# Optimization experiments

Measured on AMD Instinct MI355X. Metric: run time of the kernel, lower is better.

The kernel has to match this reference:

```python
import jax, jax.numpy as jnp
import numpy as np

N = 50000; E = 800000; B = 5000
ND = 32; ED = 16; HD = 64; H = 128; L = 3
IN_DIM = ND + 2 * H  # 288, GNN in_channels
NEG = 0.2  # GATv2 leaky_relu slope
EPS = 1e-5  # LayerNorm eps


def silu(x):
    return x * jax.nn.sigmoid(x)


def layer_norm(x, g, b):
    mu = jnp.mean(x, -1, keepdims=True)
    v = jnp.var(x, -1, keepdims=True)
    return (x - mu) * jax.lax.rsqrt(v + EPS) * g + b


def setup_inputs() -> dict:
    key = jax.random.key(0)
    ks = iter(jax.random.split(key, 48))

    def w(shape):
        return jax.random.normal(next(ks), shape, jnp.float32) * 0.02

    inp = {}
    inp['x_t'] = jax.random.normal(next(ks), (N, ND), jnp.float32)
    inp['t'] = jax.random.randint(next(ks), (N,), 0, 1000)
    inp['household_features'] = jax.random.normal(next(ks), (B, HD), jnp.float32)
    inp['edge_index'] = jax.random.randint(next(ks), (2, E), 0, N)
    inp['edge_attr'] = jax.random.normal(next(ks), (E, ED), jnp.float32)
    inp['batch'] = jnp.sort(jax.random.randint(next(ks), (N,), 0, B))
    z = jnp.zeros; o = jnp.ones
    inp.update(dict(
        tW1=w((1, H)), tb1=z(H), tW2=w((H, H)), tb2=z(H),
        hW1=w((HD, H)), hb1=z(H), hg1=o(H), hB1=z(H),
        hW2=w((H, H)), hb2=z(H), hg2=o(H), hB2=z(H),
        Wl=w((L, IN_DIM, H)), bl=z((L, H)), Wr=w((L, IN_DIM, H)), br=z((L, H)),
        We=w((L, ED, H)), att=w((L, H)), gb=z((L, H)),
        fcpW=w((H, IN_DIM)), fcpb=z(IN_DIM),
        npW1=w((H, H)), npb1=z(H), npg=o(H), npB=z(H),
        npW2=w((H, ND)), npb2=z(ND)))
    return inp


def reference(x_t, t, household_features, edge_index, edge_attr, batch,
              tW1, tb1, tW2, tb2,
              hW1, hb1, hg1, hB1, hW2, hb2, hg2, hB2,
              Wl, bl, Wr, br, We, att, gb,
              fcpW, fcpb, npW1, npb1, npg, npB, npW2, npb2):
    # time embedding: Linear(1,H) -> SiLU -> Linear(H,H)
    t_emb = silu(t[:, None].astype(jnp.float32) @ tW1 + tb1) @ tW2 + tb2
    # household encoder: (Linear, LN, SiLU) x2, then gather per node
    h = silu(layer_norm(household_features @ hW1 + hb1, hg1, hB1))
    h = silu(layer_norm(h @ hW2 + hb2, hg2, hB2))
    x = jnp.concatenate([x_t, t_emb, h[batch]], axis=1)  # [N, IN_DIM]

    # add self loops (PyG default), edge_attr filled with per-feature mean
    loop = jnp.arange(N)
    src = jnp.concatenate([edge_index[0], loop])
    dst = jnp.concatenate([edge_index[1], loop])
    ea = jnp.concatenate([edge_attr, jnp.broadcast_to(edge_attr.mean(0), (N, ED))], axis=0)

    for l in range(L):  # GATv2Conv layers (heads=1)
        xl = x @ Wl[l] + bl[l]  # [N, H] source transform
        xr = x @ Wr[l] + br[l]  # [N, H] target transform
        m = jax.nn.leaky_relu(xl[src] + xr[dst] + ea @ We[l], NEG)  # [Etot, H]
        score = m @ att[l]  # [Etot]
        smax = jax.ops.segment_max(score, dst, num_segments=N)
        ex = jnp.exp(score - smax[dst])
        denom = jax.ops.segment_sum(ex, dst, num_segments=N) + 1e-16
        alpha = ex / denom[dst]
        out = jax.ops.segment_sum(alpha[:, None] * xl[src], dst, num_segments=N) + gb[l]
        x = silu(out)
        if l < L - 1:
            x = x @ fcpW + fcpb  # fc_projection back to IN_DIM
    # node_projection: Linear, LN, SiLU, Linear
    return silu(layer_norm(x @ npW1 + npb1, npg, npB)) @ npW2 + npb2
```

## Files before the change

kernel.cpp:

```cpp
#include <hip/hip_runtime.h>
#include <hip/hip_bf16.h>

#define NN 50000
#define NE 800000
#define NB 5000
#define ND 32
#define EDD 16
#define HDD 64
#define H 128
#define ETOT (NE + NN)
#define NEG 0.2f
#define EPS_LN 1e-5f

__device__ __forceinline__ float siluf(float x){ return x / (1.f + __expf(-x)); }

__device__ __forceinline__ float wsum(float v){
  v += __shfl_xor(v, 32, 64);
  v += __shfl_xor(v, 16, 64);
  v += __shfl_xor(v, 8, 64);
  v += __shfl_xor(v, 4, 64);
  v += __shfl_xor(v, 2, 64);
  v += __shfl_xor(v, 1, 64);
  return v;
}

__device__ __forceinline__ float blockLN128(float x, const float* g, const float* b, int j, float* red){
  int lane = j & 63, wid = j >> 6;
  float s = wsum(x);
  if (lane == 0) red[wid] = s;
  __syncthreads();
  float mu = (red[0] + red[1]) * 0.0078125f;
  float d = x - mu;
  float s2 = wsum(d * d);
  if (lane == 0) red[2 + wid] = s2;
  __syncthreads();
  float var = (red[2] + red[3]) * 0.0078125f;
  return d * (1.f / sqrtf(var + EPS_LN)) * g[j] + b[j];
}

__global__ __launch_bounds__(128) void k_house(const float* __restrict__ hf,
    const float* __restrict__ hW1, const float* __restrict__ hb1,
    const float* __restrict__ hg1, const float* __restrict__ hB1,
    const float* __restrict__ hW2, const float* __restrict__ hb2,
    const float* __restrict__ hg2, const float* __restrict__ hB2,
    float* __restrict__ hout){
  __shared__ float sin_[HDD];
  __shared__ float smid[H];
  __shared__ float red[4];
  int bidx = blockIdx.x, j = threadIdx.x;
  if (j < HDD) sin_[j] = hf[bidx * HDD + j];
  __syncthreads();
  float acc = hb1[j];
  #pragma unroll
  for (int k = 0; k < HDD; k++) acc += sin_[k] * hW1[k * H + j];
  float v = siluf(blockLN128(acc, hg1, hB1, j, red));
  __syncthreads();
  smid[j] = v;
  __syncthreads();
  float acc2 = hb2[j];
  #pragma unroll
  for (int k = 0; k < H; k++) acc2 += smid[k] * hW2[k * H + j];
  float v2 = siluf(blockLN128(acc2, hg2, hB2, j, red));
  hout[bidx * H + j] = v2;
}

__global__ __launch_bounds__(128) void k_temb(const float* __restrict__ tW1, const float* __restrict__ tb1,
    const float* __restrict__ tW2, const float* __restrict__ tb2, float* __restrict__ table){
  __shared__ float smid[H];
  int bidx = blockIdx.x, j = threadIdx.x;
  float tv = (float)bidx;
  smid[j] = siluf(tv * tW1[j] + tb1[j]);
  __syncthreads();
  float acc = tb2[j];
  #pragma unroll
  for (int k = 0; k < H; k++) acc += smid[k] * tW2[k * H + j];
  table[bidx * H + j] = acc;
}

__global__ __launch_bounds__(256) void k_gemm(const float* __restrict__ A, const float* __restrict__ W,
    const float* __restrict__ bias, float* __restrict__ C, int M, int K, int Nc){
  __shared__ float As[16][68];
  __shared__ float Ws[16][64];
  int t = threadIdx.x;
  int m0 = blockIdx.x * 64, n0 = blockIdx.y * 64;
  int tx = t & 15, ty = t >> 4;
  int la_m = t >> 2, la_k = (t & 3) << 2;
  int lw_k = t >> 4, lw_j = (t & 15) << 2;
  float acc[4][4] = {{0.f}};
  int arow = m0 + la_m;
  for (int k0 = 0; k0 < K; k0 += 16){
    float4 a = make_float4(0.f, 0.f, 0.f, 0.f);
    if (arow < M) a = *(const float4*)(A + (size_t)arow * K + k0 + la_k);
    As[la_k + 0][la_m] = a.x; As[la_k + 1][la_m] = a.y;
    As[la_k + 2][la_m] = a.z; As[la_k + 3][la_m] = a.w;
    float4 wv = make_float4(0.f, 0.f, 0.f, 0.f);
    if (n0 + lw_j < Nc) wv = *(const float4*)(W + (size_t)(k0 + lw_k) * Nc + n0 + lw_j);
    *(float4*)&Ws[lw_k][lw_j] = wv;
    __syncthreads();
    #pragma unroll
    for (int k = 0; k < 16; k++){
      float4 a4 = *(const float4*)&As[k][ty << 2];
      float4 b4 = *(const float4*)&Ws[k][tx << 2];
      acc[0][0] += a4.x * b4.x; acc[0][1] += a4.x * b4.y; acc[0][2] += a4.x * b4.z; acc[0][3] += a4.x * b4.w;
      acc[1][0] += a4.y * b4.x; acc[1][1] += a4.y * b4.y; acc[1][2] += a4.y * b4.z; acc[1][3] += a4.y * b4.w;
      acc[2][0] += a4.z * b4.x; acc[2][1] += a4.z * b4.y; acc[2][2] += a4.z * b4.z; acc[2][3] += a4.z * b4.w;
      acc[3][0] += a4.w * b4.x; acc[3][1] += a4.w * b4.y; acc[3][2] += a4.w * b4.z; acc[3][3] += a4.w * b4.w;
    }
    __syncthreads();
  }
  int col = n0 + (tx << 2);
  if (col < Nc){
    float4 b4 = make_float4(0.f, 0.f, 0.f, 0.f);
    if (bias) b4 = *(const float4*)(bias + col);
    #pragma unroll
    for (int r = 0; r < 4; r++){
      int row = m0 + (ty << 2) + r;
      if (row < M){
        float4 o = make_float4(acc[r][0] + b4.x, acc[r][1] + b4.y, acc[r][2] + b4.z, acc[r][3] + b4.w);
        *(float4*)(C + (size_t)row * Nc + col) = o;
      }
    }
  }
}

__global__ __launch_bounds__(256) void k_gemm128(const float* __restrict__ A, const float* __restrict__ W,
    const float* __restrict__ bias, float* __restrict__ C, int M, int K, int Nc){
  __shared__ float As[16][132];
  __shared__ float Ws[16][128];
  int t = threadIdx.x;
  int m0 = blockIdx.x * 128, n0 = blockIdx.y * 128;
  int tx = t & 15, ty = t >> 4;
  float acc[8][8];
  #pragma unroll
  for (int r = 0; r < 8; r++)
    #pragma unroll
    for (int c = 0; c < 8; c++) acc[r][c] = 0.f;
  for (int k0 = 0; k0 < K; k0 += 16){
    #pragma unroll
    for (int l = 0; l < 2; l++){
      int idx = t + l * 256;
      int ar = idx >> 2, ac = (idx & 3) << 2;
      float4 a = make_float4(0.f, 0.f, 0.f, 0.f);
      if (m0 + ar < M) a = *(const float4*)(A + (size_t)(m0 + ar) * K + k0 + ac);
      As[ac + 0][ar] = a.x; As[ac + 1][ar] = a.y;
      As[ac + 2][ar] = a.z; As[ac + 3][ar] = a.w;
    }
    #pragma unroll
    for (int l = 0; l < 2; l++){
      int idx = t + l * 256;
      int wr = idx >> 5, wc = (idx & 31) << 2;
      float4 wv = make_float4(0.f, 0.f, 0.f, 0.f);
      if (n0 + wc < Nc) wv = *(const float4*)(W + (size_t)(k0 + wr) * Nc + n0 + wc);
      *(float4*)&Ws[wr][wc] = wv;
    }
    __syncthreads();
    #pragma unroll
    for (int k = 0; k < 16; k++){
      float4 a0 = *(const float4*)&As[k][ty * 8];
      float4 a1 = *(const float4*)&As[k][ty * 8 + 4];
      float4 b0 = *(const float4*)&Ws[k][tx * 8];
      float4 b1 = *(const float4*)&Ws[k][tx * 8 + 4];
      float ar_[8] = {a0.x, a0.y, a0.z, a0.w, a1.x, a1.y, a1.z, a1.w};
      float bc_[8] = {b0.x, b0.y, b0.z, b0.w, b1.x, b1.y, b1.z, b1.w};
      #pragma unroll
      for (int r = 0; r < 8; r++)
        #pragma unroll
        for (int c = 0; c < 8; c++) acc[r][c] += ar_[r] * bc_[c];
    }
    __syncthreads();
  }
  int col = n0 + tx * 8;
  float4 bb0 = make_float4(0.f, 0.f, 0.f, 0.f), bb1 = bb0;
  if (bias && col < Nc){ bb0 = *(const float4*)(bias + col); bb1 = *(const float4*)(bias + col + 4); }
  #pragma unroll
  for (int r = 0; r < 8; r++){
    int row = m0 + ty * 8 + r;
    if (row < M && col < Nc){
      float4 o0 = make_float4(acc[r][0] + bb0.x, acc[r][1] + bb0.y, acc[r][2] + bb0.z, acc[r][3] + bb0.w);
      float4 o1 = make_float4(acc[r][4] + bb1.x, acc[r][5] + bb1.y, acc[r][6] + bb1.z, acc[r][7] + bb1.w);
      *(float4*)(C + (size_t)row * Nc + col) = o0;
      *(float4*)(C + (size_t)row * Nc + col + 4) = o1;
    }
  }
}

__global__ void k_pack0(const float* __restrict__ Wl, const float* __restrict__ Wr,
    float* __restrict__ Whead, float* __restrict__ Wmid, float* __restrict__ Wtail){
  int r = blockIdx.x, c = threadIdx.x;
  float v = (c < H) ? Wl[r * H + c] : Wr[r * H + (c - H)];
  if (r < 32) Whead[r * 256 + c] = v;
  else if (r < 160) Wmid[(r - 32) * 256 + c] = v;
  else Wtail[(r - 160) * 256 + c] = v;
}
__global__ void k_packW(const float* __restrict__ Wl, const float* __restrict__ Wr, float* __restrict__ Wp){
  int r = blockIdx.x, c = threadIdx.x;
  Wp[r * 256 + c] = (c < H) ? Wl[r * H + c] : Wr[r * H + (c - H)];
}
__global__ void k_bias0(const float* __restrict__ bl, const float* __restrict__ br, float* __restrict__ b0){
  int c = threadIdx.x;
  b0[c] = (c < H) ? bl[c] : br[c - H];
}
__global__ void k_cvec(const float* __restrict__ fcpb, const float* __restrict__ Wp,
    const float* __restrict__ bl, const float* __restrict__ br, float* __restrict__ cc){
  int c = threadIdx.x;
  float acc = (c < H) ? bl[c] : br[c - H];
  for (int k = 0; k < 288; k++) acc += fcpb[k] * Wp[k * 256 + c];
  cc[c] = acc;
}

__global__ __launch_bounds__(256) void k_xlr0(const float* __restrict__ x_t, const int* __restrict__ t,
    const int* __restrict__ batch, const float* __restrict__ T0, const float* __restrict__ H0,
    const float* __restrict__ Whead, const float* __restrict__ b0, float* __restrict__ xlr){
  __shared__ float sx[ND];
  __shared__ int sti, sbi;
  int i = blockIdx.x, c = threadIdx.x;
  if (c < ND) sx[c] = x_t[i * ND + c];
  if (c == 0){ sti = t[i]; sbi = batch[i]; }
  __syncthreads();
  float acc = b0[c] + T0[(size_t)sti * 256 + c] + H0[(size_t)sbi * 256 + c];
  #pragma unroll
  for (int k = 0; k < ND; k++) acc += sx[k] * Whead[k * 256 + c];
  xlr[(size_t)i * 256 + c] = acc;
}

__global__ void k_edge_mean(const float* __restrict__ ea, float* __restrict__ sum16){
  __shared__ float ss[16];
  int t = threadIdx.x;
  if (t < 16) ss[t] = 0.f;
  __syncthreads();
  float p[16];
  #pragma unroll
  for (int k = 0; k < 16; k++) p[k] = 0.f;
  for (int r = blockIdx.x * blockDim.x + t; r < NE; r += gridDim.x * blockDim.x){
    const float4* rp = (const float4*)(ea + (size_t)r * 16);
    float4 q0 = rp[0], q1 = rp[1], q2 = rp[2], q3 = rp[3];
    p[0] += q0.x; p[1] += q0.y; p[2] += q0.z; p[3] += q0.w;
    p[4] += q1.x; p[5] += q1.y; p[6] += q1.z; p[7] += q1.w;
    p[8] += q2.x; p[9] += q2.y; p[10] += q2.z; p[11] += q2.w;
    p[12] += q3.x; p[13] += q3.y; p[14] += q3.z; p[15] += q3.w;
  }
  #pragma unroll
  for (int k = 0; k < 16; k++) atomicAdd(&ss[k], p[k]);
  __syncthreads();
  if (t < 16) atomicAdd(&sum16[t], ss[t]);
}
__global__ void k_mean_scale(float* sum16){
  sum16[threadIdx.x] *= (1.f / NE);
}

__global__ void k_deg_init(int* __restrict__ deg){
  int i = blockIdx.x * 256 + threadIdx.x;
  if (i < NN) deg[i] = 1;
}
__global__ void k_deg_count(const int* __restrict__ eidx, int* __restrict__ deg){
  int e = blockIdx.x * 256 + threadIdx.x;
  if (e < NE) atomicAdd(&deg[eidx[NE + e]], 1);
}
__global__ __launch_bounds__(256) void k_scan1(const int* __restrict__ deg, int* __restrict__ row_ptr, int* __restrict__ bs){
  __shared__ int sc[256];
  int t = threadIdx.x;
  int base = blockIdx.x * 1024 + t * 4;
  int v0 = (base + 0 < NN) ? deg[base + 0] : 0;
  int v1 = (base + 1 < NN) ? deg[base + 1] : 0;
  int v2 = (base + 2 < NN) ? deg[base + 2] : 0;
  int v3 = (base + 3 < NN) ? deg[base + 3] : 0;
  int s0 = v0, s1 = s0 + v1, s2 = s1 + v2, s3 = s2 + v3;
  sc[t] = s3;
  __syncthreads();
  for (int off = 1; off < 256; off <<= 1){
    int add = (t >= off) ? sc[t - off] : 0;
    __syncthreads();
    sc[t] += add;
    __syncthreads();
  }
  int excl = sc[t] - s3;
  if (base + 0 < NN) row_ptr[base + 1] = excl + s0;
  if (base + 1 < NN) row_ptr[base + 2] = excl + s1;
  if (base + 2 < NN) row_ptr[base + 3] = excl + s2;
  if (base + 3 < NN) row_ptr[base + 4] = excl + s3;
  if (t == 255) bs[blockIdx.x] = sc[255];
}
__global__ void k_scan2(int* __restrict__ bs, int nb){
  int lane = threadIdx.x;
  int v = (lane < nb) ? bs[lane] : 0;
  for (int off = 1; off < 64; off <<= 1){
    int n = __shfl_up(v, off, 64);
    if (lane >= off) v += n;
  }
  if (lane < nb) bs[lane] = v;
}
__global__ void k_scan3(int* __restrict__ row_ptr, const int* __restrict__ bs){
  int i = blockIdx.x * 256 + threadIdx.x;
  if (i == 0) row_ptr[0] = 0;
  if (i < NN){
    int chunk = i >> 10;
    if (chunk > 0) row_ptr[i + 1] += bs[chunk - 1];
  }
}
__global__ void k_fill_init(const int* __restrict__ row_ptr, int* __restrict__ fill){
  int i = blockIdx.x * 256 + threadIdx.x;
  if (i < NN) fill[i] = row_ptr[i];
}
__global__ void k_fill_edges(const int* __restrict__ eidx, int* __restrict__ fill,
    int* __restrict__ csrc, int* __restrict__ ceid){
  int e = blockIdx.x * 256 + threadIdx.x;
  if (e < NE){
    int d = eidx[NE + e];
    int pos = atomicAdd(&fill[d], 1);
    csrc[pos] = eidx[e];
    ceid[pos] = e;
  }
}
__global__ void k_fill_self(int* __restrict__ fill, int* __restrict__ csrc, int* __restrict__ ceid){
  int i = blockIdx.x * 256 + threadIdx.x;
  if (i < NN){
    int pos = atomicAdd(&fill[i], 1);
    csrc[pos] = i;
    ceid[pos] = NE;
  }
}

__global__ __launch_bounds__(256) void k_sagg(const float* __restrict__ xlr,
    const float* __restrict__ ea, const float* __restrict__ eamean,
    const float* __restrict__ Wel, const float* __restrict__ attl, const float* __restrict__ gbl,
    const int* __restrict__ row_ptr, const int* __restrict__ csrc, const int* __restrict__ ceid,
    float* __restrict__ y){
  int t = threadIdx.x;
  int wid = t >> 6, lane = t & 63;
  int i = blockIdx.x * 4 + wid;
  if (i >= NN) return;
  int dim = lane << 1;
  float2 rW[16];
  #pragma unroll
  for (int k = 0; k < 16; k++) rW[k] = *(const float2*)(Wel + k * H + dim);
  float2 xr = *(const float2*)(xlr + (size_t)i * 256 + H + dim);
  float a0 = attl[dim], a1 = attl[dim + 1];
  int row = __builtin_amdgcn_readfirstlane(row_ptr[i]);
  int end = __builtin_amdgcn_readfirstlane(row_ptr[i + 1]);
  float m = -1e30f, den = 0.f, ax = 0.f, ay = 0.f;
  int s_c = __builtin_amdgcn_readfirstlane(csrc[row]);
  int e_c = __builtin_amdgcn_readfirstlane(ceid[row]);
  float2 vl_c = *(const float2*)(xlr + (size_t)s_c * 256 + dim);
  const float* ep_c = (e_c < NE) ? (ea + (size_t)e_c * 16) : eamean;
  float4 q0 = *(const float4*)(ep_c);
  float4 q1 = *(const float4*)(ep_c + 4);
  float4 q2 = *(const float4*)(ep_c + 8);
  float4 q3 = *(const float4*)(ep_c + 12);
  for (int p = row; p < end; ++p){
    int pn = (p + 1 < end) ? (p + 1) : p;
    int s_n = __builtin_amdgcn_readfirstlane(csrc[pn]);
    int e_n = __builtin_amdgcn_readfirstlane(ceid[pn]);
    float2 vl_n = *(const float2*)(xlr + (size_t)s_n * 256 + dim);
    const float* ep_n = (e_n < NE) ? (ea + (size_t)e_n * 16) : eamean;
    float4 n0 = *(const float4*)(ep_n);
    float4 n1 = *(const float4*)(ep_n + 4);
    float4 n2 = *(const float4*)(ep_n + 8);
    float4 n3 = *(const float4*)(ep_n + 12);
    float eav[16] = {q0.x, q0.y, q0.z, q0.w, q1.x, q1.y, q1.z, q1.w,
                     q2.x, q2.y, q2.z, q2.w, q3.x, q3.y, q3.z, q3.w};
    float ew0 = 0.f, ew1 = 0.f;
    #pragma unroll
    for (int k = 0; k < 16; k++){ ew0 += eav[k] * rW[k].x; ew1 += eav[k] * rW[k].y; }
    float vx = vl_c.x + xr.x + ew0;
    float vy = vl_c.y + xr.y + ew1;
    vx = fmaxf(vx, NEG * vx);
    vy = fmaxf(vy, NEG * vy);
    float sc = wsum(a0 * vx + a1 * vy);
    if (sc <= m){
      float wv = __expf(sc - m);
      den += wv; ax += wv * vl_c.x; ay += wv * vl_c.y;
    } else {
      float scale = __expf(m - sc);
      den = den * scale + 1.f;
      ax = ax * scale + vl_c.x;
      ay = ay * scale + vl_c.y;
      m = sc;
    }
    vl_c = vl_n; q0 = n0; q1 = n1; q2 = n2; q3 = n3;
  }
  float inv = 1.f / (den + 1e-16f);
  float ox = siluf(ax * inv + gbl[dim]);
  float oy = siluf(ay * inv + gbl[dim + 1]);
  *(float2*)(y + (size_t)i * H + dim) = make_float2(ox, oy);
}

__global__ __launch_bounds__(128) void k_ln_silu(const float* __restrict__ z, const float* __restrict__ g,
    const float* __restrict__ b, float* __restrict__ z2){
  __shared__ float red[4];
  int i = blockIdx.x, j = threadIdx.x;
  float x = z[(size_t)i * H + j];
  float v = blockLN128(x, g, b, j, red);
  z2[(size_t)i * H + j] = siluf(v);
}

extern "C" void kernel_launch(void* const* d_in, const int* in_sizes, int n_in,
                              void* d_out, int out_size, void* d_ws, size_t ws_size,
                              hipStream_t stream){
  (void)in_sizes; (void)n_in; (void)out_size; (void)ws_size;
  const float* x_t  = (const float*)d_in[0];
  const int*   t    = (const int*)d_in[1];
  const float* hf   = (const float*)d_in[2];
  const int*   eidx = (const int*)d_in[3];
  const float* ea   = (const float*)d_in[4];
  const int*   batch= (const int*)d_in[5];
  const float* tW1  = (const float*)d_in[6];
  const float* tb1  = (const float*)d_in[7];
  const float* tW2  = (const float*)d_in[8];
  const float* tb2  = (const float*)d_in[9];
  const float* hW1  = (const float*)d_in[10];
  const float* hb1  = (const float*)d_in[11];
  const float* hg1  = (const float*)d_in[12];
  const float* hB1  = (const float*)d_in[13];
  const float* hW2  = (const float*)d_in[14];
  const float* hb2  = (const float*)d_in[15];
  const float* hg2  = (const float*)d_in[16];
  const float* hB2  = (const float*)d_in[17];
  const float* Wl   = (const float*)d_in[18];
  const float* bl   = (const float*)d_in[19];
  const float* Wr   = (const float*)d_in[20];
  const float* br   = (const float*)d_in[21];
  const float* We   = (const float*)d_in[22];
  const float* att  = (const float*)d_in[23];
  const float* gb   = (const float*)d_in[24];
  const float* fcpW = (const float*)d_in[25];
  const float* fcpb = (const float*)d_in[26];
  const float* npW1 = (const float*)d_in[27];
  const float* npb1 = (const float*)d_in[28];
  const float* npg  = (const float*)d_in[29];
  const float* npB  = (const float*)d_in[30];
  const float* npW2 = (const float*)d_in[31];
  const float* npb2 = (const float*)d_in[32];

  char* w = (char*)d_ws;
  size_t off = 0;
  auto alloc = [&](size_t bytes) -> void* {
    void* p = w + off;
    off += (bytes + 255) & ~(size_t)255;
    return p;
  };
  float* table = (float*)alloc((size_t)1000 * H * 4);
  float* hbuf  = (float*)alloc((size_t)NB * H * 4);
  float* T0    = (float*)alloc((size_t)1000 * 256 * 4);
  float* H0b   = (float*)alloc((size_t)NB * 256 * 4);
  float* W0h   = (float*)alloc((size_t)32 * 256 * 4);
  float* W0m   = (float*)alloc((size_t)128 * 256 * 4);
  float* W0t   = (float*)alloc((size_t)128 * 256 * 4);
  float* b0    = (float*)alloc(256 * 4);
  float* Wp1   = (float*)alloc((size_t)288 * 256 * 4);
  float* Wp2   = (float*)alloc((size_t)288 * 256 * 4);
  float* Ac1   = (float*)alloc((size_t)128 * 256 * 4);
  float* Ac2   = (float*)alloc((size_t)128 * 256 * 4);
  float* cc1   = (float*)alloc(256 * 4);
  float* cc2   = (float*)alloc(256 * 4);
  float* eam   = (float*)alloc(16 * 4);
  int* deg     = (int*)alloc((size_t)NN * 4);
  int* row_ptr = (int*)alloc((size_t)(NN + 1) * 4);
  int* fill    = (int*)alloc((size_t)NN * 4);
  int* bs      = (int*)alloc(64 * 4);
  int* csrc    = (int*)alloc((size_t)ETOT * 4);
  int* ceid    = (int*)alloc((size_t)ETOT * 4);
  float* xlr   = (float*)alloc((size_t)NN * 256 * 4);
  float* y     = (float*)alloc((size_t)NN * H * 4);
  float* z  = xlr;
  float* z2 = xlr + (size_t)NN * H;

  hipMemsetAsync(eam, 0, 64, stream);
  k_edge_mean<<<512, 256, 0, stream>>>(ea, eam);
  k_mean_scale<<<1, 16, 0, stream>>>(eam);
  k_house<<<NB, 128, 0, stream>>>(hf, hW1, hb1, hg1, hB1, hW2, hb2, hg2, hB2, hbuf);
  k_temb<<<1000, 128, 0, stream>>>(tW1, tb1, tW2, tb2, table);
  k_deg_init<<<(NN + 255) / 256, 256, 0, stream>>>(deg);
  k_deg_count<<<(NE + 255) / 256, 256, 0, stream>>>(eidx, deg);
  k_scan1<<<49, 256, 0, stream>>>(deg, row_ptr, bs);
  k_scan2<<<1, 64, 0, stream>>>(bs, 49);
  k_scan3<<<(NN + 255) / 256, 256, 0, stream>>>(row_ptr, bs);
  k_fill_init<<<(NN + 255) / 256, 256, 0, stream>>>(row_ptr, fill);
  k_fill_edges<<<(NE + 255) / 256, 256, 0, stream>>>(eidx, fill, csrc, ceid);
  k_fill_self<<<(NN + 255) / 256, 256, 0, stream>>>(fill, csrc, ceid);
  k_pack0<<<288, 256, 0, stream>>>(Wl, Wr, W0h, W0m, W0t);
  k_bias0<<<1, 256, 0, stream>>>(bl, br, b0);
  k_packW<<<288, 256, 0, stream>>>(Wl + 1 * 288 * H, Wr + 1 * 288 * H, Wp1);
  k_packW<<<288, 256, 0, stream>>>(Wl + 2 * 288 * H, Wr + 2 * 288 * H, Wp2);
  k_cvec<<<1, 256, 0, stream>>>(fcpb, Wp1, bl + H, br + H, cc1);
  k_cvec<<<1, 256, 0, stream>>>(fcpb, Wp2, bl + 2 * H, br + 2 * H, cc2);
  auto gemm = [&](const float* A, const float* W_, const float* bias, float* C, int M, int K, int Nc){
    dim3 g((M + 63) / 64, (Nc + 63) / 64);
    k_gemm<<<g, 256, 0, stream>>>(A, W_, bias, C, M, K, Nc);
  };
  auto gemm128 = [&](const float* A, const float* W_, const float* bias, float* C, int M, int K, int Nc){
    dim3 g((M + 127) / 128, (Nc + 127) / 128);
    k_gemm128<<<g, 256, 0, stream>>>(A, W_, bias, C, M, K, Nc);
  };
  gemm128(table, W0m, nullptr, T0, 1000, H, 256);
  gemm128(hbuf, W0t, nullptr, H0b, NB, H, 256);
  gemm(fcpW, Wp1, nullptr, Ac1, H, 288, 256);
  gemm(fcpW, Wp2, nullptr, Ac2, H, 288, 256);
  k_xlr0<<<NN, 256, 0, stream>>>(x_t, t, batch, T0, H0b, W0h, b0, xlr);
  k_sagg<<<(NN + 3) / 4, 256, 0, stream>>>(xlr, ea, eam, We, att, gb, row_ptr, csrc, ceid, y);
  gemm128(y, Ac1, cc1, xlr, NN, H, 256);
  k_sagg<<<(NN + 3) / 4, 256, 0, stream>>>(xlr, ea, eam, We + 16 * H, att + H, gb + H, row_ptr, csrc, ceid, y);
  gemm128(y, Ac2, cc2, xlr, NN, H, 256);
  k_sagg<<<(NN + 3) / 4, 256, 0, stream>>>(xlr, ea, eam, We + 32 * H, att + 2 * H, gb + 2 * H, row_ptr, csrc, ceid, y);
  gemm128(y, npW1, npb1, z, NN, H, H);
  k_ln_silu<<<NN, 128, 0, stream>>>(z, npg, npB, z2);
  gemm(z2, npW2, npb2, (float*)d_out, NN, H, ND);
}
```

Baseline: 1.059 ms.

## Fuse setup kernels, fuse final GEMM with LayerNorm+SiLU, rework edge aggregation

```diff
diff --git a/kernel.cpp b/kernel.cpp
--- a/kernel.cpp
+++ b/kernel.cpp
@@ -12,6 +12,8 @@
 #define NEG 0.2f
 #define EPS_LN 1e-5f
 
+typedef float pf2 __attribute__((ext_vector_type(2)));
+
 __device__ __forceinline__ float siluf(float x){ return x / (1.f + __expf(-x)); }
 
 __device__ __forceinline__ float wsum(float v){
@@ -22,6 +24,18 @@
   v += __shfl_xor(v, 2, 64);
   v += __shfl_xor(v, 1, 64);
   return v;
+}
+
+#define DPP_ADD(v, ctrl) \
+  v += __builtin_bit_cast(float, __builtin_amdgcn_update_dpp(0, __builtin_bit_cast(int, v), ctrl, 0xf, 0xf, true))
+__device__ __forceinline__ float wsum_bcast(float v){
+  DPP_ADD(v, 0x111);
+  DPP_ADD(v, 0x112);
+  DPP_ADD(v, 0x114);
+  DPP_ADD(v, 0x118);
+  DPP_ADD(v, 0x142);
+  DPP_ADD(v, 0x143);
+  return __builtin_bit_cast(float, __builtin_amdgcn_readlane(__builtin_bit_cast(int, v), 63));
 }
 
 __device__ __forceinline__ float blockLN128(float x, const float* g, const float* b, int j, float* red){
@@ -184,43 +198,142 @@
   }
 }
 
-__global__ void k_pack0(const float* __restrict__ Wl, const float* __restrict__ Wr,
-    float* __restrict__ Whead, float* __restrict__ Wmid, float* __restrict__ Wtail){
-  int r = blockIdx.x, c = threadIdx.x;
-  float v = (c < H) ? Wl[r * H + c] : Wr[r * H + (c - H)];
-  if (r < 32) Whead[r * 256 + c] = v;
-  else if (r < 160) Wmid[(r - 32) * 256 + c] = v;
-  else Wtail[(r - 160) * 256 + c] = v;
-}
-__global__ void k_packW(const float* __restrict__ Wl, const float* __restrict__ Wr, float* __restrict__ Wp){
-  int r = blockIdx.x, c = threadIdx.x;
-  Wp[r * 256 + c] = (c < H) ? Wl[r * H + c] : Wr[r * H + (c - H)];
-}
-__global__ void k_bias0(const float* __restrict__ bl, const float* __restrict__ br, float* __restrict__ b0){
-  int c = threadIdx.x;
-  b0[c] = (c < H) ? bl[c] : br[c - H];
-}
-__global__ void k_cvec(const float* __restrict__ fcpb, const float* __restrict__ Wp,
-    const float* __restrict__ bl, const float* __restrict__ br, float* __restrict__ cc){
-  int c = threadIdx.x;
-  float acc = (c < H) ? bl[c] : br[c - H];
-  for (int k = 0; k < 288; k++) acc += fcpb[k] * Wp[k * 256 + c];
-  cc[c] = acc;
-}
-
-__global__ __launch_bounds__(256) void k_xlr0(const float* __restrict__ x_t, const int* __restrict__ t,
+__global__ __launch_bounds__(256) void k_gemmln(const float* __restrict__ A, const float* __restrict__ W,
+    const float* __restrict__ bias, const float* __restrict__ g, const float* __restrict__ B,
+    float* __restrict__ out, int M){
+  __shared__ float As[16][132];
+  __shared__ float Ws[16][128];
+  int t = threadIdx.x;
+  int m0 = blockIdx.x * 128;
+  int tx = t & 15, ty = t >> 4;
+  float acc[8][8];
+  #pragma unroll
+  for (int r = 0; r < 8; r++)
+    #pragma unroll
+    for (int c = 0; c < 8; c++) acc[r][c] = 0.f;
+  for (int k0 = 0; k0 < H; k0 += 16){
+    #pragma unroll
+    for (int l = 0; l < 2; l++){
+      int idx = t + l * 256;
+      int ar = idx >> 2, ac = (idx & 3) << 2;
+      float4 a = make_float4(0.f, 0.f, 0.f, 0.f);
+      if (m0 + ar < M) a = *(const float4*)(A + (size_t)(m0 + ar) * H + k0 + ac);
+      As[ac + 0][ar] = a.x; As[ac + 1][ar] = a.y;
+      As[ac + 2][ar] = a.z; As[ac + 3][ar] = a.w;
+    }
+    #pragma unroll
+    for (int l = 0; l < 2; l++){
+      int idx = t + l * 256;
+      int wr = idx >> 5, wc = (idx & 31) << 2;
+      *(float4*)&Ws[wr][wc] = *(const float4*)(W + (size_t)(k0 + wr) * H + wc);
+    }
+    __syncthreads();
+    #pragma unroll
+    for (int k = 0; k < 16; k++){
+      float4 a0 = *(const float4*)&As[k][ty * 8];
+      float4 a1 = *(const float4*)&As[k][ty * 8 + 4];
+      float4 b0 = *(const float4*)&Ws[k][tx * 8];
+      float4 b1 = *(const float4*)&Ws[k][tx * 8 + 4];
+      float ar_[8] = {a0.x, a0.y, a0.z, a0.w, a1.x, a1.y, a1.z, a1.w};
+      float bc_[8] = {b0.x, b0.y, b0.z, b0.w, b1.x, b1.y, b1.z, b1.w};
+      #pragma unroll
+      for (int r = 0; r < 8; r++)
+        #pragma unroll
+        for (int c = 0; c < 8; c++) acc[r][c] += ar_[r] * bc_[c];
+    }
+    __syncthreads();
+  }
+  int col = tx * 8;
+  float bb[8], gv[8], Bv[8];
+  *(float4*)&bb[0] = *(const float4*)(bias + col); *(float4*)&bb[4] = *(const float4*)(bias + col + 4);
+  *(float4*)&gv[0] = *(const float4*)(g + col);    *(float4*)&gv[4] = *(const float4*)(g + col + 4);
+  *(float4*)&Bv[0] = *(const float4*)(B + col);    *(float4*)&Bv[4] = *(const float4*)(B + col + 4);
+  #pragma unroll
+  for (int r = 0; r < 8; r++){
+    int row = m0 + ty * 8 + r;
+    if (row >= M) continue;
+    float v[8];
+    float s = 0.f;
+    #pragma unroll
+    for (int c = 0; c < 8; c++){ v[c] = acc[r][c] + bb[c]; s += v[c]; }
+    s += __shfl_xor(s, 1, 16); s += __shfl_xor(s, 2, 16);
+    s += __shfl_xor(s, 4, 16); s += __shfl_xor(s, 8, 16);
+    float mu = s * 0.0078125f;
+    float s2 = 0.f;
+    #pragma unroll
+    for (int c = 0; c < 8; c++){ v[c] -= mu; s2 += v[c] * v[c]; }
+    s2 += __shfl_xor(s2, 1, 16); s2 += __shfl_xor(s2, 2, 16);
+    s2 += __shfl_xor(s2, 4, 16); s2 += __shfl_xor(s2, 8, 16);
+    float rstd = 1.f / sqrtf(s2 * 0.0078125f + EPS_LN);
+    float o[8];
+    #pragma unroll
+    for (int c = 0; c < 8; c++) o[c] = siluf(v[c] * rstd * gv[c] + Bv[c]);
+    *(float4*)(out + (size_t)row * H + col) = *(float4*)&o[0];
+    *(float4*)(out + (size_t)row * H + col + 4) = *(float4*)&o[4];
+  }
+}
+
+__global__ void k_packs(const float* __restrict__ Wl, const float* __restrict__ Wr,
+    float* __restrict__ W0h, float* __restrict__ W0m, float* __restrict__ W0t,
+    float* __restrict__ Wp1, float* __restrict__ Wp2){
+  int r = blockIdx.x, L = blockIdx.y, c = threadIdx.x;
+  float v = (c < H) ? Wl[(size_t)L * 288 * H + r * H + c] : Wr[(size_t)L * 288 * H + r * H + (c - H)];
+  if (L == 0){
+    if (r < 32) W0h[r * 256 + c] = v;
+    else if (r < 160) W0m[(r - 32) * 256 + c] = v;
+    else W0t[(r - 160) * 256 + c] = v;
+  } else {
+    (L == 1 ? Wp1 : Wp2)[r * 256 + c] = v;
+  }
+}
+__global__ void k_small(const float* __restrict__ bl, const float* __restrict__ br,
+    const float* __restrict__ Wl, const float* __restrict__ Wr, const float* __restrict__ fcpb,
+    float* __restrict__ b0, float* __restrict__ cc1, float* __restrict__ cc2, float* __restrict__ eam){
+  int c = threadIdx.x, which = blockIdx.x;
+  if (which == 0){
+    b0[c] = (c < H) ? bl[c] : br[c - H];
+    if (c < 16) eam[c] *= (1.f / NE);
+  } else {
+    int cc = (c < H) ? c : c - H;
+    const float* Wsrc = ((c < H) ? Wl : Wr) + (size_t)which * 288 * H;
+    float acc = (c < H) ? bl[which * H + cc] : br[which * H + cc];
+    for (int k = 0; k < 288; k++) acc += fcpb[k] * Wsrc[k * H + cc];
+    (which == 1 ? cc1 : cc2)[c] = acc;
+  }
+}
+
+__global__ __launch_bounds__(256) void k_xlr0(const float* __restrict__ x_t, const int* __restrict__ tt,
     const int* __restrict__ batch, const float* __restrict__ T0, const float* __restrict__ H0,
     const float* __restrict__ Whead, const float* __restrict__ b0, float* __restrict__ xlr){
-  __shared__ float sx[ND];
-  __shared__ int sti, sbi;
-  int i = blockIdx.x, c = threadIdx.x;
-  if (c < ND) sx[c] = x_t[i * ND + c];
-  if (c == 0){ sti = t[i]; sbi = batch[i]; }
-  __syncthreads();
-  float acc = b0[c] + T0[(size_t)sti * 256 + c] + H0[(size_t)sbi * 256 + c];
-  #pragma unroll
-  for (int k = 0; k < ND; k++) acc += sx[k] * Whead[k * 256 + c];
-  xlr[(size_t)i * 256 + c] = acc;
+  __shared__ float sx[4][ND];
+  __shared__ int sti[4], sbi[4];
+  int b4 = blockIdx.x * 4;
+  int t = threadIdx.x;
+  if (t < 128){
+    int n = t >> 5, k = t & 31;
+    int i = b4 + n;
+    if (i < NN) sx[n][k] = x_t[(size_t)i * ND + k];
+  }
+  if (t < 4){
+    int i = b4 + t;
+    if (i < NN){ sti[t] = tt[i]; sbi[t] = batch[i]; }
+  }
+  __syncthreads();
+  int wid = t >> 6, lane = t & 63;
+  int i = b4 + wid;
+  if (i >= NN) return;
+  int c = lane << 2;
+  float4 acc = *(const float4*)(b0 + c);
+  float4 tv = *(const float4*)(T0 + (size_t)sti[wid] * 256 + c);
+  float4 hv = *(const float4*)(H0 + (size_t)sbi[wid] * 256 + c);
+  acc.x += tv.x + hv.x; acc.y += tv.y + hv.y; acc.z += tv.z + hv.z; acc.w += tv.w + hv.w;
+  #pragma unroll
+  for (int k = 0; k < ND; k++){
+    float xk = sx[wid][k];
+    float4 wv = *(const float4*)(Whead + k * 256 + c);
+    acc.x += xk * wv.x; acc.y += xk * wv.y; acc.z += xk * wv.z; acc.w += xk * wv.w;
+  }
+  *(float4*)(xlr + (size_t)i * 256 + c) = acc;
 }
 
 __global__ void k_edge_mean(const float* __restrict__ ea, float* __restrict__ sum16){
@@ -244,14 +357,7 @@
   __syncthreads();
   if (t < 16) atomicAdd(&sum16[t], ss[t]);
 }
-__global__ void k_mean_scale(float* sum16){
-  sum16[threadIdx.x] *= (1.f / NE);
-}
-
-__global__ void k_deg_init(int* __restrict__ deg){
-  int i = blockIdx.x * 256 + threadIdx.x;
-  if (i < NN) deg[i] = 1;
-}
+
 __global__ void k_deg_count(const int* __restrict__ eidx, int* __restrict__ deg){
   int e = blockIdx.x * 256 + threadIdx.x;
   if (e < NE) atomicAdd(&deg[eidx[NE + e]], 1);
@@ -260,10 +366,10 @@
   __shared__ int sc[256];
   int t = threadIdx.x;
   int base = blockIdx.x * 1024 + t * 4;
-  int v0 = (base + 0 < NN) ? deg[base + 0] : 0;
-  int v1 = (base + 1 < NN) ? deg[base + 1] : 0;
-  int v2 = (base + 2 < NN) ? deg[base + 2] : 0;
-  int v3 = (base + 3 < NN) ? deg[base + 3] : 0;
+  int v0 = (base + 0 < NN) ? deg[base + 0] + 1 : 0;
+  int v1 = (base + 1 < NN) ? deg[base + 1] + 1 : 0;
+  int v2 = (base + 2 < NN) ? deg[base + 2] + 1 : 0;
+  int v3 = (base + 3 < NN) ? deg[base + 3] + 1 : 0;
   int s0 = v0, s1 = s0 + v1, s2 = s1 + v2, s3 = s2 + v3;
   sc[t] = s3;
   __syncthreads();
@@ -289,17 +395,16 @@
   }
   if (lane < nb) bs[lane] = v;
 }
-__global__ void k_scan3(int* __restrict__ row_ptr, const int* __restrict__ bs){
+__global__ void k_scan3(int* __restrict__ row_ptr, const int* __restrict__ bs,
+    const int* __restrict__ deg, int* __restrict__ fill){
   int i = blockIdx.x * 256 + threadIdx.x;
   if (i == 0) row_ptr[0] = 0;
   if (i < NN){
     int chunk = i >> 10;
-    if (chunk > 0) row_ptr[i + 1] += bs[chunk - 1];
-  }
-}
-__global__ void k_fill_init(const int* __restrict__ row_ptr, int* __restrict__ fill){
-  int i = blockIdx.x * 256 + threadIdx.x;
-  if (i < NN) fill[i] = row_ptr[i];
+    int rp1 = row_ptr[i + 1] + ((chunk > 0) ? bs[chunk - 1] : 0);
+    row_ptr[i + 1] = rp1;
+    fill[i] = rp1 - deg[i] - 1;
+  }
 }
 __global__ void k_fill_edges(const int* __restrict__ eidx, int* __restrict__ fill,
     int* __restrict__ csrc, int* __restrict__ ceid){
@@ -330,67 +435,45 @@
   int i = blockIdx.x * 4 + wid;
   if (i >= NN) return;
   int dim = lane << 1;
-  float2 rW[16];
-  #pragma unroll
-  for (int k = 0; k < 16; k++) rW[k] = *(const float2*)(Wel + k * H + dim);
-  float2 xr = *(const float2*)(xlr + (size_t)i * 256 + H + dim);
-  float a0 = attl[dim], a1 = attl[dim + 1];
+  pf2 rW[16];
+  #pragma unroll
+  for (int k = 0; k < 16; k++) rW[k] = *(const pf2*)(Wel + k * H + dim);
+  pf2 xr2 = *(const pf2*)(xlr + (size_t)i * 256 + H + dim);
+  pf2 a2 = *(const pf2*)(attl + dim);
   int row = __builtin_amdgcn_readfirstlane(row_ptr[i]);
   int end = __builtin_amdgcn_readfirstlane(row_ptr[i + 1]);
-  float m = -1e30f, den = 0.f, ax = 0.f, ay = 0.f;
-  int s_c = __builtin_amdgcn_readfirstlane(csrc[row]);
-  int e_c = __builtin_amdgcn_readfirstlane(ceid[row]);
-  float2 vl_c = *(const float2*)(xlr + (size_t)s_c * 256 + dim);
-  const float* ep_c = (e_c < NE) ? (ea + (size_t)e_c * 16) : eamean;
-  float4 q0 = *(const float4*)(ep_c);
-  float4 q1 = *(const float4*)(ep_c + 4);
-  float4 q2 = *(const float4*)(ep_c + 8);
-  float4 q3 = *(const float4*)(ep_c + 12);
+  float m = -1e30f, den = 0.f;
+  pf2 acc2; acc2.x = 0.f; acc2.y = 0.f;
   for (int p = row; p < end; ++p){
-    int pn = (p + 1 < end) ? (p + 1) : p;
-    int s_n = __builtin_amdgcn_readfirstlane(csrc[pn]);
-    int e_n = __builtin_amdgcn_readfirstlane(ceid[pn]);
-    float2 vl_n = *(const float2*)(xlr + (size_t)s_n * 256 + dim);
-    const float* ep_n = (e_n < NE) ? (ea + (size_t)e_n * 16) : eamean;
-    float4 n0 = *(const float4*)(ep_n);
-    float4 n1 = *(const float4*)(ep_n + 4);
-    float4 n2 = *(const float4*)(ep_n + 8);
-    float4 n3 = *(const float4*)(ep_n + 12);
-    float eav[16] = {q0.x, q0.y, q0.z, q0.w, q1.x, q1.y, q1.z, q1.w,
-                     q2.x, q2.y, q2.z, q2.w, q3.x, q3.y, q3.z, q3.w};
-    float ew0 = 0.f, ew1 = 0.f;
-    #pragma unroll
-    for (int k = 0; k < 16; k++){ ew0 += eav[k] * rW[k].x; ew1 += eav[k] * rW[k].y; }
-    float vx = vl_c.x + xr.x + ew0;
-    float vy = vl_c.y + xr.y + ew1;
-    vx = fmaxf(vx, NEG * vx);
-    vy = fmaxf(vy, NEG * vy);
-    float sc = wsum(a0 * vx + a1 * vy);
+    int s   = __builtin_amdgcn_readfirstlane(csrc[p]);
+    int eid = __builtin_amdgcn_readfirstlane(ceid[p]);
+    pf2 vl = *(const pf2*)(xlr + (size_t)s * 256 + dim);
+    const float* ep = (eid < NE) ? (ea + (size_t)eid * 16) : eamean;
+    pf2 ew; ew.x = 0.f; ew.y = 0.f;
+    #pragma unroll
+    for (int k = 0; k < 16; k++) ew += rW[k] * ep[k];
+    pf2 vv = vl + xr2 + ew;
+    pf2 vn = vv * NEG;
+    vv.x = fmaxf(vv.x, vn.x);
+    vv.y = fmaxf(vv.y, vn.y);
+    pf2 sp = a2 * vv;
+    float sc = wsum_bcast(sp.x + sp.y);
     if (sc <= m){
       float wv = __expf(sc - m);
-      den += wv; ax += wv * vl_c.x; ay += wv * vl_c.y;
+      den += wv;
+      acc2 += vl * wv;
     } else {
       float scale = __expf(m - sc);
       den = den * scale + 1.f;
-      ax = ax * scale + vl_c.x;
-      ay = ay * scale + vl_c.y;
+      acc2 = acc2 * scale + vl;
       m = sc;
     }
-    vl_c = vl_n; q0 = n0; q1 = n1; q2 = n2; q3 = n3;
   }
   float inv = 1.f / (den + 1e-16f);
-  float ox = siluf(ax * inv + gbl[dim]);
-  float oy = siluf(ay * inv + gbl[dim + 1]);
-  *(float2*)(y + (size_t)i * H + dim) = make_float2(ox, oy);
-}
-
-__global__ __launch_bounds__(128) void k_ln_silu(const float* __restrict__ z, const float* __restrict__ g,
-    const float* __restrict__ b, float* __restrict__ z2){
-  __shared__ float red[4];
-  int i = blockIdx.x, j = threadIdx.x;
-  float x = z[(size_t)i * H + j];
-  float v = blockLN128(x, g, b, j, red);
-  z2[(size_t)i * H + j] = siluf(v);
+  pf2 gb2 = *(const pf2*)(gbl + dim);
+  pf2 o = acc2 * inv + gb2;
+  o.x = siluf(o.x); o.y = siluf(o.y);
+  *(pf2*)(y + (size_t)i * H + dim) = o;
 }
 
 extern "C" void kernel_launch(void* const* d_in, const int* in_sizes, int n_in,
@@ -461,28 +544,21 @@
   int* ceid    = (int*)alloc((size_t)ETOT * 4);
   float* xlr   = (float*)alloc((size_t)NN * 256 * 4);
   float* y     = (float*)alloc((size_t)NN * H * 4);
-  float* z  = xlr;
-  float* z2 = xlr + (size_t)NN * H;
+  float* z2 = xlr;
 
   hipMemsetAsync(eam, 0, 64, stream);
+  hipMemsetAsync(deg, 0, (size_t)NN * 4, stream);
   k_edge_mean<<<512, 256, 0, stream>>>(ea, eam);
-  k_mean_scale<<<1, 16, 0, stream>>>(eam);
+  k_small<<<3, 256, 0, stream>>>(bl, br, Wl, Wr, fcpb, b0, cc1, cc2, eam);
   k_house<<<NB, 128, 0, stream>>>(hf, hW1, hb1, hg1, hB1, hW2, hb2, hg2, hB2, hbuf);
   k_temb<<<1000, 128, 0, stream>>>(tW1, tb1, tW2, tb2, table);
-  k_deg_init<<<(NN + 255) / 256, 256, 0, stream>>>(deg);
   k_deg_count<<<(NE + 255) / 256, 256, 0, stream>>>(eidx, deg);
   k_scan1<<<49, 256, 0, stream>>>(deg, row_ptr, bs);
   k_scan2<<<1, 64, 0, stream>>>(bs, 49);
-  k_scan3<<<(NN + 255) / 256, 256, 0, stream>>>(row_ptr, bs);
-  k_fill_init<<<(NN + 255) / 256, 256, 0, stream>>>(row_ptr, fill);
+  k_scan3<<<(NN + 255) / 256, 256, 0, stream>>>(row_ptr, bs, deg, fill);
   k_fill_edges<<<(NE + 255) / 256, 256, 0, stream>>>(eidx, fill, csrc, ceid);
   k_fill_self<<<(NN + 255) / 256, 256, 0, stream>>>(fill, csrc, ceid);
-  k_pack0<<<288, 256, 0, stream>>>(Wl, Wr, W0h, W0m, W0t);
-  k_bias0<<<1, 256, 0, stream>>>(bl, br, b0);
-  k_packW<<<288, 256, 0, stream>>>(Wl + 1 * 288 * H, Wr + 1 * 288 * H, Wp1);
-  k_packW<<<288, 256, 0, stream>>>(Wl + 2 * 288 * H, Wr + 2 * 288 * H, Wp2);
-  k_cvec<<<1, 256, 0, stream>>>(fcpb, Wp1, bl + H, br + H, cc1);
-  k_cvec<<<1, 256, 0, stream>>>(fcpb, Wp2, bl + 2 * H, br + 2 * H, cc2);
+  k_packs<<<dim3(288, 3), 256, 0, stream>>>(Wl, Wr, W0h, W0m, W0t, Wp1, Wp2);
   auto gemm = [&](const float* A, const float* W_, const float* bias, float* C, int M, int K, int Nc){
     dim3 g((M + 63) / 64, (Nc + 63) / 64);
     k_gemm<<<g, 256, 0, stream>>>(A, W_, bias, C, M, K, Nc);
@@ -495,13 +571,12 @@
   gemm128(hbuf, W0t, nullptr, H0b, NB, H, 256);
   gemm(fcpW, Wp1, nullptr, Ac1, H, 288, 256);
   gemm(fcpW, Wp2, nullptr, Ac2, H, 288, 256);
-  k_xlr0<<<NN, 256, 0, stream>>>(x_t, t, batch, T0, H0b, W0h, b0, xlr);
+  k_xlr0<<<(NN + 3) / 4, 256, 0, stream>>>(x_t, t, batch, T0, H0b, W0h, b0, xlr);
   k_sagg<<<(NN + 3) / 4, 256, 0, stream>>>(xlr, ea, eam, We, att, gb, row_ptr, csrc, ceid, y);
   gemm128(y, Ac1, cc1, xlr, NN, H, 256);
   k_sagg<<<(NN + 3) / 4, 256, 0, stream>>>(xlr, ea, eam, We + 16 * H, att + H, gb + H, row_ptr, csrc, ceid, y);
   gemm128(y, Ac2, cc2, xlr, NN, H, 256);
   k_sagg<<<(NN + 3) / 4, 256, 0, stream>>>(xlr, ea, eam, We + 32 * H, att + 2 * H, gb + 2 * H, row_ptr, csrc, ceid, y);
-  gemm128(y, npW1, npb1, z, NN, H, H);
-  k_ln_silu<<<NN, 128, 0, stream>>>(z, npg, npB, z2);
+  k_gemmln<<<(NN + 127) / 128, 256, 0, stream>>>(y, npW1, npb1, npg, npB, z2, NN);
   gemm(z2, npW2, npb2, (float*)d_out, NN, H, ND);
 }
```

Measured after the change: 959.1 us. 9.4% less time.
